# Optimization experiments

Hardware: AMD Instinct MI355X
Metric: run time of the kernel (lower is better)

Reference implementation:

```python
import jax, jax.numpy as jnp
import numpy as np

V = 10000   # vocab_size
L = 12      # n_layer
H = 12      # n_head
C = 768     # n_embd
TE = 64     # t_embd
WTE = C - TE
BS = 1024   # block_size
B, T = 4, 1024
D = C // H
EPS = 1e-5


def setup_inputs() -> dict:
    key = jax.random.key(0)
    ks = jax.random.split(key, 12)
    s = 0.02
    def n(k, shape, extra=1.0):
        return jax.random.normal(k, shape, jnp.float32) * (s * extra)
    resid_scale = 1.0 / np.sqrt(2 * L)  # c_proj init std scaling from _init_weights loop
    return {
        'idx': jax.random.randint(ks[0], (B, T), 0, V),
        'ts': jax.random.uniform(ks[1], (B, T), jnp.float32) * 100.0,
        'wte': n(ks[2], (V, WTE)),
        'basis_freq': jnp.asarray(1.0 / 10 ** np.linspace(0, 9, TE), jnp.float32),
        'phase': jnp.zeros((TE,), jnp.float32),
        'wpe': n(ks[3], (BS, C)),
        'ln1_w': jnp.ones((L, C), jnp.float32), 'ln1_b': jnp.zeros((L, C), jnp.float32),
        'qkv_w': n(ks[4], (L, 3 * C, C)), 'qkv_b': jnp.zeros((L, 3 * C), jnp.float32),
        'proj_w': n(ks[5], (L, C, C), resid_scale), 'proj_b': jnp.zeros((L, C), jnp.float32),
        'ln2_w': jnp.ones((L, C), jnp.float32), 'ln2_b': jnp.zeros((L, C), jnp.float32),
        'fc_w': n(ks[6], (L, 4 * C, C)), 'fc_b': jnp.zeros((L, 4 * C), jnp.float32),
        'fc2_w': n(ks[7], (L, C, 4 * C), resid_scale), 'fc2_b': jnp.zeros((L, C), jnp.float32),
        'lnf_w': jnp.ones((C,), jnp.float32), 'lnf_b': jnp.zeros((C,), jnp.float32),
        'lm_w': n(ks[8], (V, C)),
        'tp_w': n(ks[9], (1, C)),
    }


def _ln(x, w, b):
    mu = jnp.mean(x, -1, keepdims=True)
    var = jnp.mean((x - mu) ** 2, -1, keepdims=True)
    return (x - mu) * jax.lax.rsqrt(var + EPS) * w + b


def reference(idx, ts, wte, basis_freq, phase, wpe, ln1_w, ln1_b, qkv_w, qkv_b,
              proj_w, proj_b, ln2_w, ln2_b, fc_w, fc_b, fc2_w, fc2_b,
              lnf_w, lnf_b, lm_w, tp_w):
    Bv, Tv = idx.shape
    tok = wte[idx]                                      # [B,T,C-TE]
    tim = jnp.cos(ts[..., None] * basis_freq + phase)   # TimeEncode -> [B,T,TE]
    x = jnp.concatenate([tok, tim], axis=-1) + wpe[:Tv]
    mask = jnp.tril(jnp.ones((Tv, Tv), bool))
    scale = 1.0 / np.sqrt(D)

    def block(x, p):
        l1w, l1b, qw, qb, pw, pb, l2w, l2b, fw, fb, f2w, f2b = p
        h = _ln(x, l1w, l1b)
        qkv = h @ qw.T + qb                              # [B,T,3C]
        q, k, v = jnp.split(qkv, 3, axis=-1)
        def heads(z):
            return z.reshape(Bv, Tv, H, D).transpose(0, 2, 1, 3)  # [B,H,T,D]
        q, k, v = heads(q), heads(k), heads(v)
        att = jnp.einsum('bhtd,bhsd->bhts', q, k) * scale
        att = jnp.where(mask, att, -jnp.inf)             # causal masked_fill
        att = jax.nn.softmax(att, axis=-1)
        y = jnp.einsum('bhts,bhsd->bhtd', att, v)
        y = y.transpose(0, 2, 1, 3).reshape(Bv, Tv, C)
        x = x + (y @ pw.T + pb)
        h2 = _ln(x, l2w, l2b)
        m = jax.nn.gelu(h2 @ fw.T + fb, approximate=False)  # torch nn.GELU default is exact
        x = x + (m @ f2w.T + f2b)
        return x, None

    x, _ = jax.lax.scan(block, x, (ln1_w, ln1_b, qkv_w, qkv_b, proj_w, proj_b,
                                   ln2_w, ln2_b, fc_w, fc_b, fc2_w, fc2_b))
    x = _ln(x, lnf_w, lnf_b)
    logits = x @ lm_w.T          # [B,T,V]
    tpred = x @ tp_w.T           # [B,T,1]
    return logits, tpred
```

## Files before the change

kernel.cpp:

```cpp
#include <hip/hip_runtime.h>
#include <hip/hip_bf16.h>
#include <math.h>

#define Bb   4
#define Tt   1024
#define Cc   768
#define Hh   12
#define Dd   64
#define Ll   12
#define Vv   10000
#define WTEe 704
#define MTOT 4096

#define QSCALE 0.18033688f

typedef __bf16 bf16x8 __attribute__((ext_vector_type(8)));
typedef float  f32x4  __attribute__((ext_vector_type(4)));
typedef unsigned short u16;

typedef const __attribute__((address_space(1))) void* gptr_t;
typedef __attribute__((address_space(3))) void* lptr_t;

__device__ inline void gload16(const void* g, void* l) {
    __builtin_amdgcn_global_load_lds((gptr_t)g, (lptr_t)l, 16, 0, 0);
}

__device__ inline u16 f2bf(float f) {
    unsigned int u = __float_as_uint(f);
    return (u16)((u + 0x7fffu + ((u >> 16) & 1u)) >> 16);
}
__device__ inline float bf2f(u16 u) { return __uint_as_float(((unsigned)u) << 16); }

__device__ inline float gelu_f(float v) {
    float t = v * (0.797884561f + 0.0356774081f * v * v);
    float e = __expf(2.f * t);
    float th = 1.f - 2.f / (e + 1.f);
    return 0.5f * v * (1.f + th);
}

#if __has_builtin(__builtin_amdgcn_exp2f)
__device__ inline float fast_exp2(float x) { return __builtin_amdgcn_exp2f(x); }
#else
__device__ inline float fast_exp2(float x) { return exp2f(x); }
#endif

#define WAITVM(N)  asm volatile("s_waitcnt vmcnt(" #N ")" ::: "memory")
#define WAITLGKM0() asm volatile("s_waitcnt lgkmcnt(0)" ::: "memory")
#define SCHEDB()   __builtin_amdgcn_sched_barrier(0)
#define SBAR()     __builtin_amdgcn_s_barrier()

__global__ __launch_bounds__(256)
void convert_pack(const float* __restrict__ in, u16* __restrict__ out,
                  int nk8, int K, int rowmod, int scaleLim)
{
    int i = blockIdx.x * 256 + threadIdx.x;
    if (i >= nk8) return;
    int row = (i << 3) / K;
    int col = (i << 3) % K;
    float s = 1.f;
    if (rowmod && (row % rowmod) < scaleLim) s = QSCALE;
    float4 v0 = ((const float4*)in)[2 * i];
    float4 v1 = ((const float4*)in)[2 * i + 1];
    uint4 o;
    o.x = (unsigned)f2bf(v0.x * s) | ((unsigned)f2bf(v0.y * s) << 16);
    o.y = (unsigned)f2bf(v0.z * s) | ((unsigned)f2bf(v0.w * s) << 16);
    o.z = (unsigned)f2bf(v1.x * s) | ((unsigned)f2bf(v1.y * s) << 16);
    o.w = (unsigned)f2bf(v1.z * s) | ((unsigned)f2bf(v1.w * s) << 16);
    int tile = row >> 4, kt = col >> 5;
    int l = (row & 15) | (((col >> 3) & 3) << 4);
    size_t off = (((size_t)tile * (K >> 5) + kt) << 9) + l * 8;
    *(uint4*)(out + off) = o;
}

__global__ __launch_bounds__(256)
void scale_qkvb(const float* __restrict__ in, float* __restrict__ out, int n)
{
    int i = blockIdx.x * 256 + threadIdx.x;
    if (i >= n) return;
    int col = i % (3 * Cc);
    out[i] = in[i] * (col < Cc ? QSCALE : 1.f);
}

__global__ __launch_bounds__(256)
void embed_kernel(const int* __restrict__ idx, const float* __restrict__ ts,
                  const float* __restrict__ wte, const float* __restrict__ freq,
                  const float* __restrict__ ph, const float* __restrict__ wpe,
                  float* __restrict__ x)
{
    const int bt  = blockIdx.x;
    const int t   = bt & (Tt - 1);
    const int tok = idx[bt];
    const float tv = ts[bt];
#pragma unroll
    for (int j = 0; j < 3; ++j) {
        int c = threadIdx.x + (j << 8);
        float val;
        if (c < WTEe) val = wte[(size_t)tok * WTEe + c];
        else {
            int e = c - WTEe;
            val = cosf(tv * freq[e] + ph[e]);
        }
        x[(size_t)bt * Cc + c] = val + wpe[(size_t)t * Cc + c];
    }
}

__global__ __launch_bounds__(256)
void ln_pack16(const float* __restrict__ x, const float* __restrict__ wt,
               const float* __restrict__ bs, u16* __restrict__ out)
{
    __shared__ float mus[16], rss[16];
    const int tid  = threadIdx.x;
    const int lane = tid & 63;
    const int w    = tid >> 6;
    const int tile = blockIdx.x;
    const int r0   = tile << 4;

#pragma unroll
    for (int rr = 0; rr < 4; ++rr) {
        const int row = r0 + w * 4 + rr;
        const float* xr = x + (size_t)row * Cc;
        float s = 0.f, s2 = 0.f;
#pragma unroll
        for (int j = 0; j < 12; ++j) {
            float v = xr[lane + (j << 6)];
            s += v; s2 += v * v;
        }
#pragma unroll
        for (int m = 32; m; m >>= 1) {
            s  += __shfl_xor(s, m);
            s2 += __shfl_xor(s2, m);
        }
        if (lane == 0) {
            float mu = s * (1.f / 768.f);
            float var = s2 * (1.f / 768.f) - mu * mu;
            mus[w * 4 + rr] = mu;
            rss[w * 4 + rr] = rsqrtf(var + 1e-5f);
        }
    }
    __syncthreads();

    u16* ob = out + ((size_t)tile * 24 << 9);
#pragma unroll
    for (int it = 0; it < 6; ++it) {
        int c   = tid + (it << 8);
        int kt  = c >> 6, l = c & 63;
        int row = l & 15, g = l >> 4;
        int col = kt * 32 + g * 8;
        float mu = mus[row], rs = rss[row];
        const float* xp = x + (size_t)(r0 + row) * Cc + col;
        float4 a = *(const float4*)xp;
        float4 bq = *(const float4*)(xp + 4);
        ushort o[8];
        o[0] = f2bf((a.x - mu) * rs * wt[col]     + bs[col]);
        o[1] = f2bf((a.y - mu) * rs * wt[col + 1] + bs[col + 1]);
        o[2] = f2bf((a.z - mu) * rs * wt[col + 2] + bs[col + 2]);
        o[3] = f2bf((a.w - mu) * rs * wt[col + 3] + bs[col + 3]);
        o[4] = f2bf((bq.x - mu) * rs * wt[col + 4] + bs[col + 4]);
        o[5] = f2bf((bq.y - mu) * rs * wt[col + 5] + bs[col + 5]);
        o[6] = f2bf((bq.z - mu) * rs * wt[col + 6] + bs[col + 6]);
        o[7] = f2bf((bq.w - mu) * rs * wt[col + 7] + bs[col + 7]);
        *(uint4*)(ob + ((size_t)kt << 9) + l * 8) = *(uint4*)o;
    }
}

__device__ inline void st_out(float* p, size_t o, float v) { p[o] = v; }
__device__ inline void st_out(u16*   p, size_t o, float v) { p[o] = f2bf(v); }

template<int EPI, int APK, typename OutT>
__global__ __launch_bounds__(256)
void gemm_bf16(const u16* __restrict__ A, const u16* __restrict__ Wp,
               const float* __restrict__ bias, const float* __restrict__ resid,
               OutT* __restrict__ out, u16* __restrict__ vt, int N, int K)
{
    __shared__ uint4 AF[3][8][64];
    __shared__ uint4 BF[3][8][64];
    const int tid  = threadIdx.x;
    const int lane = tid & 63;
    const int w    = tid >> 6;
    const int wr   = w >> 1, wc = w & 1;
    const int lq   = lane & 15, g = lane >> 4;
    const int m0   = blockIdx.x * 128, n0 = blockIdx.y * 128;
    const int KB   = K >> 5;

    const u16 *ap0, *ap1;
    if (APK) {
        ap0 = A + ((((size_t)(m0 >> 4) + 2 * w) * KB) << 9) + lane * 8;
        ap1 = ap0 + ((size_t)KB << 9);
    } else {
        ap0 = A + (size_t)(m0 + (2 * w) * 16 + lq) * K + g * 8;
        ap1 = ap0 + (size_t)16 * K;
    }

    int tn0 = (n0 >> 4) + 2 * w, tn1 = tn0 + 1;
    const int tmax = (N >> 4) - 1;
    tn0 = tn0 < tmax ? tn0 : tmax;
    tn1 = tn1 < tmax ? tn1 : tmax;
    const u16* bq0 = Wp + (((size_t)tn0 * KB) << 9) + lane * 8;
    const u16* bq1 = Wp + (((size_t)tn1 * KB) << 9) + lane * 8;

    f32x4 acc[4][4] = {};
    const int nk = KB;

#define GSTAGE(s, sl) do {                                               \
        if (APK) {                                                       \
            gload16(ap0 + ((size_t)(s) << 9), &AF[sl][2 * w][lane]);     \
            gload16(ap1 + ((size_t)(s) << 9), &AF[sl][2 * w + 1][lane]); \
        } else {                                                         \
            gload16(ap0 + ((s) << 5), &AF[sl][2 * w][lane]);             \
            gload16(ap1 + ((s) << 5), &AF[sl][2 * w + 1][lane]);         \
        }                                                                \
        gload16(bq0 + ((size_t)(s) << 9), &BF[sl][2 * w][lane]);         \
        gload16(bq1 + ((size_t)(s) << 9), &BF[sl][2 * w + 1][lane]); } while (0)

    GSTAGE(0, 0);
    GSTAGE(1, 1);
    WAITVM(4);
    SCHEDB();
    SBAR();
    SCHEDB();

    int sl = 0;
    for (int t = 0; t < nk; ++t) {
        int sl2 = sl + 2; if (sl2 >= 3) sl2 -= 3;
        if (t + 2 < nk) GSTAGE(t + 2, sl2);

        bf16x8 af[4], bfr[4];
#pragma unroll
        for (int mi = 0; mi < 4; ++mi)
            af[mi] = __builtin_bit_cast(bf16x8, AF[sl][wr * 4 + mi][lane]);
#pragma unroll
        for (int ni = 0; ni < 4; ++ni)
            bfr[ni] = __builtin_bit_cast(bf16x8, BF[sl][wc * 4 + ni][lane]);
        __builtin_amdgcn_s_setprio(1);
#pragma unroll
        for (int mi = 0; mi < 4; ++mi)
#pragma unroll
            for (int ni = 0; ni < 4; ++ni)
                acc[mi][ni] = __builtin_amdgcn_mfma_f32_16x16x32_bf16(
                    af[mi], bfr[ni], acc[mi][ni], 0, 0, 0);
        __builtin_amdgcn_s_setprio(0);

        if (t + 2 < nk) { WAITVM(4); }
        else           { WAITVM(0); }
        SCHEDB();
        SBAR();
        SCHEDB();
        sl = (sl + 1 == 3) ? 0 : sl + 1;
    }
#undef GSTAGE

    if (EPI == 3 && n0 >= 1536) {
#pragma unroll
        for (int mi = 0; mi < 4; ++mi)
#pragma unroll
            for (int ni = 0; ni < 4; ++ni) {
                int col = n0 + wc * 64 + ni * 16 + lq;
                int c2  = col - 1536;
                int hh  = c2 >> 6, dd = c2 & 63;
                int row = m0 + wr * 64 + mi * 16 + g * 4;
                int bb  = row >> 10, tr = row & 1023;
                float bv = bias[col];
                ushort4 o;
                o.x = f2bf(acc[mi][ni][0] + bv);
                o.y = f2bf(acc[mi][ni][1] + bv);
                o.z = f2bf(acc[mi][ni][2] + bv);
                o.w = f2bf(acc[mi][ni][3] + bv);
                *(ushort4*)&vt[(((size_t)bb * Hh + hh) * Dd + dd) * Tt + tr] = o;
            }
        return;
    }

#pragma unroll
    for (int mi = 0; mi < 4; ++mi)
#pragma unroll
        for (int ni = 0; ni < 4; ++ni) {
            int col = n0 + wc * 64 + ni * 16 + lq;
            if (col >= N) continue;
            int row = m0 + wr * 64 + mi * 16 + g * 4;
            float bv = bias ? bias[col] : 0.f;
#pragma unroll
            for (int q = 0; q < 4; ++q) {
                float v = acc[mi][ni][q] + bv;
                size_t o = (size_t)(row + q) * N + col;
                if (EPI == 1) v += resid[o];
                if (EPI == 2) v = gelu_f(v);
                st_out(out, o, v);
            }
        }
}

template<int EPI, typename OutT>
__global__ __launch_bounds__(256)
void gemm_n64(const u16* __restrict__ A, const u16* __restrict__ Wp,
              const float* __restrict__ bias, const float* __restrict__ resid,
              OutT* __restrict__ out, int N, int K)
{
    __shared__ uint4 AF[2][8][64];
    __shared__ uint4 BF[2][16][64];
    const int tid  = threadIdx.x;
    const int lane = tid & 63;
    const int w    = tid >> 6;
    const int wr   = w & 1, wc = w >> 1;
    const int lq   = lane & 15, g = lane >> 4;
    const int m0   = blockIdx.x * 64, n0 = blockIdx.y * 128;
    const int KB   = K >> 5;
    const int nk   = K >> 6;

    const u16* ap = A + (size_t)(m0 + w * 16 + lq) * K + g * 8;
    int tn0 = (n0 >> 4) + 2 * w, tn1 = tn0 + 1;
    const int tmax = (N >> 4) - 1;
    tn0 = tn0 < tmax ? tn0 : tmax;
    tn1 = tn1 < tmax ? tn1 : tmax;
    const u16* bq0 = Wp + (((size_t)tn0 * KB) << 9) + lane * 8;
    const u16* bq1 = Wp + (((size_t)tn1 * KB) << 9) + lane * 8;

    f32x4 acc[2][4] = {};

#define GSTAGE(t, bi) do {                                                 \
        gload16(ap + ((t) << 6),      &AF[bi][2 * w][lane]);               \
        gload16(ap + ((t) << 6) + 32, &AF[bi][2 * w + 1][lane]);           \
        gload16(bq0 + ((size_t)(2 * (t)) << 9),     &BF[bi][4 * w][lane]); \
        gload16(bq0 + ((size_t)(2 * (t) + 1) << 9), &BF[bi][4 * w + 1][lane]); \
        gload16(bq1 + ((size_t)(2 * (t)) << 9),     &BF[bi][4 * w + 2][lane]); \
        gload16(bq1 + ((size_t)(2 * (t) + 1) << 9), &BF[bi][4 * w + 3][lane]); } while (0)

    GSTAGE(0, 0);
    WAITVM(0);
    SCHEDB();
    SBAR();
    SCHEDB();

    for (int t = 0; t < nk; ++t) {
        const int buf = t & 1;
        if (t + 1 < nk) GSTAGE(t + 1, buf ^ 1);

#pragma unroll
        for (int s = 0; s < 2; ++s) {
            bf16x8 a0 = __builtin_bit_cast(bf16x8, AF[buf][(wr * 2) * 2 + s][lane]);
            bf16x8 a1 = __builtin_bit_cast(bf16x8, AF[buf][(wr * 2 + 1) * 2 + s][lane]);
            bf16x8 bb[4];
#pragma unroll
            for (int ni = 0; ni < 4; ++ni)
                bb[ni] = __builtin_bit_cast(bf16x8, BF[buf][(wc * 4 + ni) * 2 + s][lane]);
            __builtin_amdgcn_s_setprio(1);
#pragma unroll
            for (int ni = 0; ni < 4; ++ni) {
                acc[0][ni] = __builtin_amdgcn_mfma_f32_16x16x32_bf16(
                    a0, bb[ni], acc[0][ni], 0, 0, 0);
                acc[1][ni] = __builtin_amdgcn_mfma_f32_16x16x32_bf16(
                    a1, bb[ni], acc[1][ni], 0, 0, 0);
            }
            __builtin_amdgcn_s_setprio(0);
        }

        WAITVM(0);
        SCHEDB();
        SBAR();
        SCHEDB();
    }
#undef GSTAGE

#pragma unroll
    for (int mi = 0; mi < 2; ++mi)
#pragma unroll
        for (int ni = 0; ni < 4; ++ni) {
            int col = n0 + wc * 64 + ni * 16 + lq;
            if (col >= N) continue;
            int row = m0 + (wr * 2 + mi) * 16 + g * 4;
            float bv = bias ? bias[col] : 0.f;
#pragma unroll
            for (int q = 0; q < 4; ++q) {
                float v = acc[mi][ni][q] + bv;
                size_t o = (size_t)(row + q) * N + col;
                if (EPI == 1) v += resid[o];
                if (EPI == 2) v = gelu_f(v);
                st_out(out, o, v);
            }
        }
}

template<int EPI, typename OutT>
__global__ __launch_bounds__(512, 2)
void gemm8p(const u16* __restrict__ Apk, const u16* __restrict__ Wp,
            const float* __restrict__ bias, const float* __restrict__ resid,
            OutT* __restrict__ out, int N, int K)
{
    __shared__ uint4 AF[2][16][2][64];
    __shared__ uint4 BF[2][16][2][64];
    const int tid  = threadIdx.x;
    const int lane = tid & 63;
    const int w    = tid >> 6;
    const int wr   = w >> 2, wc = w & 3;
    const int lq   = lane & 15, g = lane >> 4;
    const int m0   = blockIdx.x * 256, n0 = blockIdx.y * 256;
    const int KB   = K >> 5;

    const u16* aq0 = Apk + ((((size_t)(m0 >> 4) + 2 * w) * KB) << 9) + lane * 8;
    const u16* aq1 = aq0 + ((size_t)KB << 9);

    int tn0 = (n0 >> 4) + 2 * w, tn1 = tn0 + 1;
    const int tmax = (N >> 4) - 1;
    tn0 = tn0 < tmax ? tn0 : tmax;
    tn1 = tn1 < tmax ? tn1 : tmax;
    const u16* bq0 = Wp + (((size_t)tn0 * KB) << 9) + lane * 8;
    const u16* bq1 = Wp + (((size_t)tn1 * KB) << 9) + lane * 8;

    f32x4 acc[8][4] = {};
    const int nt = K >> 6;

    gload16(aq0,       &AF[0][2 * w][0][lane]);
    gload16(aq1,       &AF[0][2 * w + 1][0][lane]);
    gload16(bq0,       &BF[0][2 * w][0][lane]);
    gload16(bq1,       &BF[0][2 * w + 1][0][lane]);
    gload16(aq0 + 512, &AF[0][2 * w][1][lane]);
    gload16(aq1 + 512, &AF[0][2 * w + 1][1][lane]);
    gload16(bq0 + 512, &BF[0][2 * w][1][lane]);
    gload16(bq1 + 512, &BF[0][2 * w + 1][1][lane]);
    WAITVM(0);
    SCHEDB();
    SBAR();

    int buf = 0;
    for (int t = 0; t < nt; ++t) {
        const bool more = (t + 1 < nt);
        const size_t bb0 = (size_t)(2 * (t + 1)) << 9;
        bf16x8 a0[4], a1[4], b0[4];

#pragma unroll
        for (int i = 0; i < 4; ++i)
            a0[i] = __builtin_bit_cast(bf16x8, AF[buf][wr * 8 + i][0][lane]);
#pragma unroll
        for (int i = 0; i < 4; ++i)
            b0[i] = __builtin_bit_cast(bf16x8, BF[buf][wc * 4 + i][0][lane]);
        if (more) {
            gload16(aq0 + bb0, &AF[buf ^ 1][2 * w][0][lane]);
            gload16(aq1 + bb0, &AF[buf ^ 1][2 * w + 1][0][lane]);
        }
        SCHEDB();
        SBAR();
        WAITLGKM0();
        SCHEDB();
        __builtin_amdgcn_s_setprio(1);
#pragma unroll
        for (int mi = 0; mi < 4; ++mi)
#pragma unroll
            for (int ni = 0; ni < 4; ++ni)
                acc[mi][ni] = __builtin_amdgcn_mfma_f32_16x16x32_bf16(
                    a0[mi], b0[ni], acc[mi][ni], 0, 0, 0);
        __builtin_amdgcn_s_setprio(0);
        SBAR();

#pragma unroll
        for (int i = 0; i < 4; ++i)
            a1[i] = __builtin_bit_cast(bf16x8, AF[buf][wr * 8 + 4 + i][0][lane]);
        if (more) {
            gload16(bq0 + bb0, &BF[buf ^ 1][2 * w][0][lane]);
            gload16(bq1 + bb0, &BF[buf ^ 1][2 * w + 1][0][lane]);
        }
        SCHEDB();
        SBAR();
        WAITLGKM0();
        SCHEDB();
        __builtin_amdgcn_s_setprio(1);
#pragma unroll
        for (int mi = 0; mi < 4; ++mi)
#pragma unroll
            for (int ni = 0; ni < 4; ++ni)
                acc[4 + mi][ni] = __builtin_amdgcn_mfma_f32_16x16x32_bf16(
                    a1[mi], b0[ni], acc[4 + mi][ni], 0, 0, 0);
        __builtin_amdgcn_s_setprio(0);
        if (more) { WAITVM(4); } else { WAITVM(0); }
        SCHEDB();
        SBAR();

#pragma unroll
        for (int i = 0; i < 4; ++i)
            a0[i] = __builtin_bit_cast(bf16x8, AF[buf][wr * 8 + i][1][lane]);
#pragma unroll
        for (int i = 0; i < 4; ++i)
            b0[i] = __builtin_bit_cast(bf16x8, BF[buf][wc * 4 + i][1][lane]);
        if (more) {
            gload16(aq0 + bb0 + 512, &AF[buf ^ 1][2 * w][1][lane]);
            gload16(aq1 + bb0 + 512, &AF[buf ^ 1][2 * w + 1][1][lane]);
        }
        SCHEDB();
        SBAR();
        WAITLGKM0();
        SCHEDB();
        __builtin_amdgcn_s_setprio(1);
#pragma unroll
        for (int mi = 0; mi < 4; ++mi)
#pragma unroll
            for (int ni = 0; ni < 4; ++ni)
                acc[mi][ni] = __builtin_amdgcn_mfma_f32_16x16x32_bf16(
                    a0[mi], b0[ni], acc[mi][ni], 0, 0, 0);
        __builtin_amdgcn_s_setprio(0);
        SBAR();

#pragma unroll
        for (int i = 0; i < 4; ++i)
            a1[i] = __builtin_bit_cast(bf16x8, AF[buf][wr * 8 + 4 + i][1][lane]);
        if (more) {
            gload16(bq0 + bb0 + 512, &BF[buf ^ 1][2 * w][1][lane]);
            gload16(bq1 + bb0 + 512, &BF[buf ^ 1][2 * w + 1][1][lane]);
        }
        SCHEDB();
        SBAR();
        WAITLGKM0();
        SCHEDB();
        __builtin_amdgcn_s_setprio(1);
#pragma unroll
        for (int mi = 0; mi < 4; ++mi)
#pragma unroll
            for (int ni = 0; ni < 4; ++ni)
                acc[4 + mi][ni] = __builtin_amdgcn_mfma_f32_16x16x32_bf16(
                    a1[mi], b0[ni], acc[4 + mi][ni], 0, 0, 0);
        __builtin_amdgcn_s_setprio(0);
        if (more) { WAITVM(4); } else { WAITVM(0); }
        SCHEDB();
        SBAR();

        buf ^= 1;
    }

#pragma unroll
    for (int mi = 0; mi < 8; ++mi)
#pragma unroll
        for (int ni = 0; ni < 4; ++ni) {
            int col = n0 + wc * 64 + ni * 16 + lq;
            if (col >= N) continue;
            int row = m0 + wr * 128 + mi * 16 + g * 4;
            float bv = bias ? bias[col] : 0.f;
#pragma unroll
            for (int q = 0; q < 4; ++q) {
                float v = acc[mi][ni][q] + bv;
                size_t o = (size_t)(row + q) * N + col;
                if (EPI == 1) v += resid[o];
                if (EPI == 2) v = gelu_f(v);
                st_out(out, o, v);
            }
        }
}

__global__ __launch_bounds__(512)
void attn_mfma(const u16* __restrict__ qkv, const u16* __restrict__ vt,
               u16* __restrict__ y)
{
    __shared__ uint4 KF[2][4][2][64];
    __shared__ uint4 VF[2][4][2][64];

    const int tid  = threadIdx.x;
    const int lane = tid & 63;
    const int w    = tid >> 6;
    const int lq   = lane & 15, g = lane >> 4;
    const int m    = gridDim.x - 1 - blockIdx.x;
    const int bh   = blockIdx.y;
    const int b    = bh / Hh, h = bh % Hh;
    const int wq0  = m * 128 + w * 16;
    const size_t base = (size_t)b * Tt * (3 * Cc);

    const u16* qrow = qkv + base + (size_t)(wq0 + lq) * (3 * Cc) + h * Dd;
    bf16x8 qf0 = __builtin_bit_cast(bf16x8, *(const uint4*)(qrow + g * 8));
    bf16x8 qf1 = __builtin_bit_cast(bf16x8, *(const uint4*)(qrow + 32 + g * 8));

    f32x4 yac[4] = {};
    float lrun = 0.f;

    const int wm = w & 3;
    const u16* kbase = qkv + base + Cc + h * Dd + (size_t)(wm * 16 + lq) * (3 * Cc) + g * 8;
    const u16* vbase = vt + ((size_t)bh * Dd + wm * 16 + lq) * Tt + g * 8;

#define STAGE(c, bi)  do {                                              \
        if (w < 4) {                                                    \
            const u16* kp = kbase + (size_t)(c) * 64 * (3 * Cc);        \
            gload16(kp,      &KF[bi][wm][0][lane]);                     \
            gload16(kp + 32, &KF[bi][wm][1][lane]);                     \
        } else {                                                        \
            const u16* vp = vbase + (c) * 64;                           \
            gload16(vp,      &VF[bi][wm][0][lane]);                     \
            gload16(vp + 32, &VF[bi][wm][1][lane]);                     \
        }                                                               \
    } while (0)

    const int nch = 2 * m + 2;
    STAGE(0, 0);
    WAITVM(0);
    SCHEDB();
    SBAR();

    const int srcb = lq + ((g & 1) << 5);

    int buf = 0;
    for (int c = 0; c < nch; ++c) {
        if (c + 1 < nch) STAGE(c + 1, buf ^ 1);

        f32x4 sc[4] = {};
        __builtin_amdgcn_s_setprio(1);
#pragma unroll
        for (int nt = 0; nt < 4; ++nt) {
            bf16x8 k0 = __builtin_bit_cast(bf16x8, KF[buf][nt][0][lane]);
            bf16x8 k1 = __builtin_bit_cast(bf16x8, KF[buf][nt][1][lane]);
            sc[nt] = __builtin_amdgcn_mfma_f32_16x16x32_bf16(k0, qf0, sc[nt], 0, 0, 0);
            sc[nt] = __builtin_amdgcn_mfma_f32_16x16x32_bf16(k1, qf1, sc[nt], 0, 0, 0);
        }
        __builtin_amdgcn_s_setprio(0);

        const int s0 = c * 64;
        if (s0 + 63 > wq0) {
            const int qg = wq0 + lq;
#pragma unroll
            for (int nt = 0; nt < 4; ++nt) {
                const int kb = s0 + nt * 16 + (g << 2);
#pragma unroll
                for (int j = 0; j < 4; ++j)
                    if (kb + j > qg) sc[nt][j] = -1e30f;
            }
        }

        float ls = 0.f;
#pragma unroll
        for (int nt = 0; nt < 4; ++nt)
#pragma unroll
            for (int j = 0; j < 4; ++j) {
                float p = fast_exp2(sc[nt][j]);
                sc[nt][j] = p;
                ls += p;
            }
        ls += __shfl_xor(ls, 16);
        ls += __shfl_xor(ls, 32);
        lrun += ls;

        unsigned pk[4][2];
#pragma unroll
        for (int nt = 0; nt < 4; ++nt) {
            unsigned u0 = __float_as_uint(sc[nt][0]);
            unsigned u1 = __float_as_uint(sc[nt][1]);
            unsigned u2 = __float_as_uint(sc[nt][2]);
            unsigned u3 = __float_as_uint(sc[nt][3]);
            pk[nt][0] = (u0 >> 16) | (u1 & 0xffff0000u);
            pk[nt][1] = (u2 >> 16) | (u3 & 0xffff0000u);
        }

        unsigned pa0[4], pa1[4];
#pragma unroll
        for (int m2 = 0; m2 < 4; ++m2) {
            int hsel = m2 & 1;
            int src  = srcb + ((m2 >> 1) << 4);
            unsigned lo0 = __shfl(pk[0][hsel], src);
            unsigned hi0 = __shfl(pk[1][hsel], src);
            unsigned lo1 = __shfl(pk[2][hsel], src);
            unsigned hi1 = __shfl(pk[3][hsel], src);
            pa0[m2] = (g >> 1) ? hi0 : lo0;
            pa1[m2] = (g >> 1) ? hi1 : lo1;
        }
        uint4 A0 = make_uint4(pa0[0], pa0[1], pa0[2], pa0[3]);
        uint4 A1 = make_uint4(pa1[0], pa1[1], pa1[2], pa1[3]);
        bf16x8 pA0 = __builtin_bit_cast(bf16x8, A0);
        bf16x8 pA1 = __builtin_bit_cast(bf16x8, A1);

        __builtin_amdgcn_s_setprio(1);
#pragma unroll
        for (int dt = 0; dt < 4; ++dt) {
            bf16x8 vb0 = __builtin_bit_cast(bf16x8, VF[buf][dt][0][lane]);
            bf16x8 vb1 = __builtin_bit_cast(bf16x8, VF[buf][dt][1][lane]);
            yac[dt] = __builtin_amdgcn_mfma_f32_16x16x32_bf16(pA0, vb0, yac[dt], 0, 0, 0);
            yac[dt] = __builtin_amdgcn_mfma_f32_16x16x32_bf16(pA1, vb1, yac[dt], 0, 0, 0);
        }
        __builtin_amdgcn_s_setprio(0);

        if (c + 1 < nch) { WAITVM(0); }
        SCHEDB();
        SBAR();
        buf ^= 1;
    }
#undef STAGE

    f32x4 rl;
#pragma unroll
    for (int j = 0; j < 4; ++j)
        rl[j] = 1.0f / __shfl(lrun, (g << 2) + j);
#pragma unroll
    for (int dt = 0; dt < 4; ++dt)
#pragma unroll
        for (int j = 0; j < 4; ++j)
            y[(size_t)(b * Tt + wq0 + (g << 2) + j) * Cc + h * Dd + dt * 16 + lq]
                = f2bf(yac[dt][j] * rl[j]);
}

__global__ __launch_bounds__(256)
void tpred_kernel(const u16* __restrict__ hp, const float* __restrict__ tp,
                  float* __restrict__ out)
{
    const int row  = blockIdx.x * 4 + (threadIdx.x >> 6);
    const int lane = threadIdx.x & 63;
    const int tile = row >> 4, r15 = row & 15;
    const u16* tb = hp + ((size_t)tile * 24 << 9);
    float s = 0.f;
#pragma unroll
    for (int j = 0; j < 12; ++j) {
        int col = lane + (j << 6);
        int kt = col >> 5, g = (col >> 3) & 3, e = col & 7;
        s += bf2f(tb[((size_t)kt << 9) + (r15 | (g << 4)) * 8 + e]) * tp[col];
    }
#pragma unroll
    for (int m = 32; m; m >>= 1) s += __shfl_xor(s, m);
    if (lane == 0) out[row] = s;
}

extern "C" void kernel_launch(void* const* d_in, const int* in_sizes, int n_in,
                              void* d_out, int out_size, void* d_ws, size_t ws_size,
                              hipStream_t stream)
{
    const int*   idx  = (const int*)d_in[0];
    const float* ts   = (const float*)d_in[1];
    const float* wte  = (const float*)d_in[2];
    const float* freq = (const float*)d_in[3];
    const float* ph   = (const float*)d_in[4];
    const float* wpe  = (const float*)d_in[5];
    const float* ln1w = (const float*)d_in[6];
    const float* ln1b = (const float*)d_in[7];
    const float* qkvw = (const float*)d_in[8];
    const float* qkvb = (const float*)d_in[9];
    const float* pw   = (const float*)d_in[10];
    const float* pb   = (const float*)d_in[11];
    const float* ln2w = (const float*)d_in[12];
    const float* ln2b = (const float*)d_in[13];
    const float* fcw  = (const float*)d_in[14];
    const float* fcb  = (const float*)d_in[15];
    const float* f2w  = (const float*)d_in[16];
    const float* f2b  = (const float*)d_in[17];
    const float* lnfw = (const float*)d_in[18];
    const float* lnfb = (const float*)d_in[19];
    const float* lmw  = (const float*)d_in[20];
    const float* tpw  = (const float*)d_in[21];
    float* out = (float*)d_out;

    const int n_qkvw = 3 * Cc * Cc, n_pw = Cc * Cc, n_fcw = 4 * Cc * Cc;

    char* p = (char*)d_ws;
    float* x    = (float*)p;               p += (size_t)MTOT * Cc * 4;
    u16*   qkvB = (u16*)p;                 p += (size_t)MTOT * 3 * Cc * 2;
    u16*   VtB  = (u16*)p;                 p += (size_t)Bb * Hh * Dd * Tt * 2;
    u16*   hB   = (u16*)p;                 p += (size_t)MTOT * Cc * 2;
    u16*   yB   = (u16*)p;                 p += (size_t)MTOT * Cc * 2;
    u16*   mbB  = (u16*)p;                 p += (size_t)MTOT * 4 * Cc * 2;
    u16*   lmwB = (u16*)p;                 p += (size_t)Vv * Cc * 2;
    float* sbias= (float*)p;               p += (size_t)Ll * 3 * Cc * 4;
    char* wbase = p;

    size_t need_big = (size_t)(wbase - (char*)d_ws)
                    + ((size_t)Ll * (n_qkvw + n_pw + 2 * n_fcw)) * 2;
    bool big = ws_size >= need_big;

    u16 *wqA, *wpA, *wfA, *wf2A;
    if (big) {
        wqA  = (u16*)wbase;                wbase += (size_t)Ll * n_qkvw * 2;
        wpA  = (u16*)wbase;                wbase += (size_t)Ll * n_pw * 2;
        wfA  = (u16*)wbase;                wbase += (size_t)Ll * n_fcw * 2;
        wf2A = (u16*)wbase;
    } else {
        wqA  = (u16*)wbase;                wbase += (size_t)n_qkvw * 2;
        wpA  = (u16*)wbase;                wbase += (size_t)n_pw * 2;
        wfA  = (u16*)wbase;                wbase += (size_t)n_fcw * 2;
        wf2A = (u16*)wbase;
    }

    auto pack = [&](const float* src, u16* dst, size_t rows, int K,
                    int rowmod, int scaleLim) {
        int nk8 = (int)(rows * K / 8);
        convert_pack<<<(nk8 + 255) / 256, 256, 0, stream>>>(
            src, dst, nk8, K, rowmod, scaleLim);
    };

    pack(lmw, lmwB, Vv, Cc, 0, 0);
    {
        int nb = Ll * 3 * Cc;
        scale_qkvb<<<(nb + 255) / 256, 256, 0, stream>>>(qkvb, sbias, nb);
    }
    if (big) {
        pack(qkvw, wqA,  (size_t)Ll * 3 * Cc, Cc, 3 * Cc, Cc);
        pack(pw,   wpA,  (size_t)Ll * Cc,     Cc, 0, 0);
        pack(fcw,  wfA,  (size_t)Ll * 4 * Cc, Cc, 0, 0);
        pack(f2w,  wf2A, (size_t)Ll * Cc, 4 * Cc, 0, 0);
    }
    embed_kernel<<<MTOT, 256, 0, stream>>>(idx, ts, wte, freq, ph, wpe, x);

    for (int l = 0; l < Ll; ++l) {
        u16 *wqB, *wpB, *wfB, *wf2B;
        if (big) {
            wqB  = wqA  + (size_t)l * n_qkvw;
            wpB  = wpA  + (size_t)l * n_pw;
            wfB  = wfA  + (size_t)l * n_fcw;
            wf2B = wf2A + (size_t)l * n_fcw;
        } else {
            wqB = wqA; wpB = wpA; wfB = wfA; wf2B = wf2A;
            pack(qkvw + (size_t)l * n_qkvw, wqB, 3 * Cc, Cc, 3 * Cc, Cc);
            pack(pw   + (size_t)l * n_pw,   wpB, Cc,     Cc, 0, 0);
            pack(fcw  + (size_t)l * n_fcw,  wfB, 4 * Cc, Cc, 0, 0);
            pack(f2w  + (size_t)l * n_fcw,  wf2B, Cc, 4 * Cc, 0, 0);
        }

        ln_pack16<<<MTOT / 16, 256, 0, stream>>>(x, ln1w + l * Cc, ln1b + l * Cc, hB);
        gemm_bf16<3, 1, u16><<<dim3(32, 18), 256, 0, stream>>>(
            hB, wqB, sbias + (size_t)l * 3 * Cc, nullptr, qkvB, VtB, 3 * Cc, Cc);
        attn_mfma<<<dim3(Tt / 128, Bb * Hh), 512, 0, stream>>>(qkvB, VtB, yB);
        gemm_n64<1, float><<<dim3(64, 6), 256, 0, stream>>>(
            yB, wpB, pb + (size_t)l * Cc, x, x, Cc, Cc);
        ln_pack16<<<MTOT / 16, 256, 0, stream>>>(x, ln2w + l * Cc, ln2b + l * Cc, hB);
        gemm_bf16<2, 1, u16><<<dim3(32, 24), 256, 0, stream>>>(
            hB, wfB, fcb + (size_t)l * 4 * Cc, nullptr, mbB, nullptr, 4 * Cc, Cc);
        gemm_n64<1, float><<<dim3(64, 6), 256, 0, stream>>>(
            mbB, wf2B, f2b + (size_t)l * Cc, x, x, Cc, 4 * Cc);
    }

    ln_pack16<<<MTOT / 16, 256, 0, stream>>>(x, lnfw, lnfb, hB);
    gemm8p<0, float><<<dim3(16, 40), 512, 0, stream>>>(
        hB, lmwB, nullptr, nullptr, out, Vv, Cc);
    tpred_kernel<<<MTOT / 4, 256, 0, stream>>>(hB, tpw, out + (size_t)MTOT * Vv);
}
```

Baseline: 2.451 ms.

## Use 64-row M tiles with 64-wide K steps for QKV and FC GEMMs

The two GEMM kernels are merged into one templated kernel with a 64x128 output tile, double-buffered 64-wide K stages, and optional packed-A input. The QKV and FC GEMMs now use this smaller tile, doubling their grid size from 128x128 tiles with a 3-stage pipeline. The goal is more blocks for better CU occupancy and load balance, at the cost of less operand reuse per block and a shallower prefetch pipeline.

```diff
diff --git a/kernel.cpp b/kernel.cpp
--- a/kernel.cpp
+++ b/kernel.cpp
@@ -168,28 +168,24 @@
 
 template<int EPI, int APK, typename OutT>
 __global__ __launch_bounds__(256)
-void gemm_bf16(const u16* __restrict__ A, const u16* __restrict__ Wp,
+void gemm_nk64(const u16* __restrict__ A, const u16* __restrict__ Wp,
                const float* __restrict__ bias, const float* __restrict__ resid,
                OutT* __restrict__ out, u16* __restrict__ vt, int N, int K)
 {
-    __shared__ uint4 AF[3][8][64];
-    __shared__ uint4 BF[3][8][64];
+    __shared__ uint4 AF[2][8][64];
+    __shared__ uint4 BF[2][16][64];
     const int tid  = threadIdx.x;
     const int lane = tid & 63;
     const int w    = tid >> 6;
-    const int wr   = w >> 1, wc = w & 1;
+    const int wr   = w & 1, wc = w >> 1;
     const int lq   = lane & 15, g = lane >> 4;
-    const int m0   = blockIdx.x * 128, n0 = blockIdx.y * 128;
+    const int m0   = blockIdx.x * 64, n0 = blockIdx.y * 128;
     const int KB   = K >> 5;
-
-    const u16 *ap0, *ap1;
-    if (APK) {
-        ap0 = A + ((((size_t)(m0 >> 4) + 2 * w) * KB) << 9) + lane * 8;
-        ap1 = ap0 + ((size_t)KB << 9);
-    } else {
-        ap0 = A + (size_t)(m0 + (2 * w) * 16 + lq) * K + g * 8;
-        ap1 = ap0 + (size_t)16 * K;
-    }
+    const int nk   = K >> 6;
+
+    const u16* ap;
+    if (APK) ap = A + ((((size_t)(m0 >> 4) + w) * KB) << 9) + lane * 8;
+    else     ap = A + (size_t)(m0 + w * 16 + lq) * K + g * 8;
 
     int tn0 = (n0 >> 4) + 2 * w, tn1 = tn0 + 1;
     const int tmax = (N >> 4) - 1;
@@ -198,66 +194,66 @@
     const u16* bq0 = Wp + (((size_t)tn0 * KB) << 9) + lane * 8;
     const u16* bq1 = Wp + (((size_t)tn1 * KB) << 9) + lane * 8;
 
-    f32x4 acc[4][4] = {};
-    const int nk = KB;
-
-#define GSTAGE(s, sl) do {                                               \
-        if (APK) {                                                       \
-            gload16(ap0 + ((size_t)(s) << 9), &AF[sl][2 * w][lane]);     \
-            gload16(ap1 + ((size_t)(s) << 9), &AF[sl][2 * w + 1][lane]); \
-        } else {                                                         \
-            gload16(ap0 + ((s) << 5), &AF[sl][2 * w][lane]);             \
-            gload16(ap1 + ((s) << 5), &AF[sl][2 * w + 1][lane]);         \
-        }                                                                \
-        gload16(bq0 + ((size_t)(s) << 9), &BF[sl][2 * w][lane]);         \
-        gload16(bq1 + ((size_t)(s) << 9), &BF[sl][2 * w + 1][lane]); } while (0)
+    f32x4 acc[2][4] = {};
+
+#define GSTAGE(t, bi) do {                                                 \
+        if (APK) {                                                         \
+            gload16(ap + ((size_t)(2 * (t)) << 9),     &AF[bi][2 * w][lane]); \
+            gload16(ap + ((size_t)(2 * (t) + 1) << 9), &AF[bi][2 * w + 1][lane]); \
+        } else {                                                           \
+            gload16(ap + ((t) << 6),      &AF[bi][2 * w][lane]);           \
+            gload16(ap + ((t) << 6) + 32, &AF[bi][2 * w + 1][lane]);       \
+        }                                                                  \
+        gload16(bq0 + ((size_t)(2 * (t)) << 9),     &BF[bi][4 * w][lane]); \
+        gload16(bq0 + ((size_t)(2 * (t) + 1) << 9), &BF[bi][4 * w + 1][lane]); \
+        gload16(bq1 + ((size_t)(2 * (t)) << 9),     &BF[bi][4 * w + 2][lane]); \
+        gload16(bq1 + ((size_t)(2 * (t) + 1) << 9), &BF[bi][4 * w + 3][lane]); } while (0)
 
     GSTAGE(0, 0);
-    GSTAGE(1, 1);
-    WAITVM(4);
+    WAITVM(0);
     SCHEDB();
     SBAR();
     SCHEDB();
 
-    int sl = 0;
     for (int t = 0; t < nk; ++t) {
-        int sl2 = sl + 2; if (sl2 >= 3) sl2 -= 3;
-        if (t + 2 < nk) GSTAGE(t + 2, sl2);
-
-        bf16x8 af[4], bfr[4];
-#pragma unroll
-        for (int mi = 0; mi < 4; ++mi)
-            af[mi] = __builtin_bit_cast(bf16x8, AF[sl][wr * 4 + mi][lane]);
-#pragma unroll
-        for (int ni = 0; ni < 4; ++ni)
-            bfr[ni] = __builtin_bit_cast(bf16x8, BF[sl][wc * 4 + ni][lane]);
-        __builtin_amdgcn_s_setprio(1);
-#pragma unroll
-        for (int mi = 0; mi < 4; ++mi)
+        const int buf = t & 1;
+        if (t + 1 < nk) GSTAGE(t + 1, buf ^ 1);
+
+#pragma unroll
+        for (int s = 0; s < 2; ++s) {
+            bf16x8 a0 = __builtin_bit_cast(bf16x8, AF[buf][(wr * 2) * 2 + s][lane]);
+            bf16x8 a1 = __builtin_bit_cast(bf16x8, AF[buf][(wr * 2 + 1) * 2 + s][lane]);
+            bf16x8 bb[4];
 #pragma unroll
             for (int ni = 0; ni < 4; ++ni)
-                acc[mi][ni] = __builtin_amdgcn_mfma_f32_16x16x32_bf16(
-                    af[mi], bfr[ni], acc[mi][ni], 0, 0, 0);
-        __builtin_amdgcn_s_setprio(0);
-
-        if (t + 2 < nk) { WAITVM(4); }
-        else           { WAITVM(0); }
-        SCHEDB();
-        SBAR();
-        SCHEDB();
-        sl = (sl + 1 == 3) ? 0 : sl + 1;
+                bb[ni] = __builtin_bit_cast(bf16x8, BF[buf][(wc * 4 + ni) * 2 + s][lane]);
+            __builtin_amdgcn_s_setprio(1);
+#pragma unroll
+            for (int ni = 0; ni < 4; ++ni) {
+                acc[0][ni] = __builtin_amdgcn_mfma_f32_16x16x32_bf16(
+                    a0, bb[ni], acc[0][ni], 0, 0, 0);
+                acc[1][ni] = __builtin_amdgcn_mfma_f32_16x16x32_bf16(
+                    a1, bb[ni], acc[1][ni], 0, 0, 0);
+            }
+            __builtin_amdgcn_s_setprio(0);
+        }
+
+        WAITVM(0);
+        SCHEDB();
+        SBAR();
+        SCHEDB();
     }
 #undef GSTAGE
 
     if (EPI == 3 && n0 >= 1536) {
 #pragma unroll
-        for (int mi = 0; mi < 4; ++mi)
+        for (int mi = 0; mi < 2; ++mi)
 #pragma unroll
             for (int ni = 0; ni < 4; ++ni) {
                 int col = n0 + wc * 64 + ni * 16 + lq;
                 int c2  = col - 1536;
                 int hh  = c2 >> 6, dd = c2 & 63;
-                int row = m0 + wr * 64 + mi * 16 + g * 4;
+                int row = m0 + (wr * 2 + mi) * 16 + g * 4;
                 int bb  = row >> 10, tr = row & 1023;
                 float bv = bias[col];
                 ushort4 o;
@@ -269,96 +265,6 @@
             }
         return;
     }
-
-#pragma unroll
-    for (int mi = 0; mi < 4; ++mi)
-#pragma unroll
-        for (int ni = 0; ni < 4; ++ni) {
-            int col = n0 + wc * 64 + ni * 16 + lq;
-            if (col >= N) continue;
-            int row = m0 + wr * 64 + mi * 16 + g * 4;
-            float bv = bias ? bias[col] : 0.f;
-#pragma unroll
-            for (int q = 0; q < 4; ++q) {
-                float v = acc[mi][ni][q] + bv;
-                size_t o = (size_t)(row + q) * N + col;
-                if (EPI == 1) v += resid[o];
-                if (EPI == 2) v = gelu_f(v);
-                st_out(out, o, v);
-            }
-        }
-}
-
-template<int EPI, typename OutT>
-__global__ __launch_bounds__(256)
-void gemm_n64(const u16* __restrict__ A, const u16* __restrict__ Wp,
-              const float* __restrict__ bias, const float* __restrict__ resid,
-              OutT* __restrict__ out, int N, int K)
-{
-    __shared__ uint4 AF[2][8][64];
-    __shared__ uint4 BF[2][16][64];
-    const int tid  = threadIdx.x;
-    const int lane = tid & 63;
-    const int w    = tid >> 6;
-    const int wr   = w & 1, wc = w >> 1;
-    const int lq   = lane & 15, g = lane >> 4;
-    const int m0   = blockIdx.x * 64, n0 = blockIdx.y * 128;
-    const int KB   = K >> 5;
-    const int nk   = K >> 6;
-
-    const u16* ap = A + (size_t)(m0 + w * 16 + lq) * K + g * 8;
-    int tn0 = (n0 >> 4) + 2 * w, tn1 = tn0 + 1;
-    const int tmax = (N >> 4) - 1;
-    tn0 = tn0 < tmax ? tn0 : tmax;
-    tn1 = tn1 < tmax ? tn1 : tmax;
-    const u16* bq0 = Wp + (((size_t)tn0 * KB) << 9) + lane * 8;
-    const u16* bq1 = Wp + (((size_t)tn1 * KB) << 9) + lane * 8;
-
-    f32x4 acc[2][4] = {};
-
-#define GSTAGE(t, bi) do {                                                 \
-        gload16(ap + ((t) << 6),      &AF[bi][2 * w][lane]);               \
-        gload16(ap + ((t) << 6) + 32, &AF[bi][2 * w + 1][lane]);           \
-        gload16(bq0 + ((size_t)(2 * (t)) << 9),     &BF[bi][4 * w][lane]); \
-        gload16(bq0 + ((size_t)(2 * (t) + 1) << 9), &BF[bi][4 * w + 1][lane]); \
-        gload16(bq1 + ((size_t)(2 * (t)) << 9),     &BF[bi][4 * w + 2][lane]); \
-        gload16(bq1 + ((size_t)(2 * (t) + 1) << 9), &BF[bi][4 * w + 3][lane]); } while (0)
-
-    GSTAGE(0, 0);
-    WAITVM(0);
-    SCHEDB();
-    SBAR();
-    SCHEDB();
-
-    for (int t = 0; t < nk; ++t) {
-        const int buf = t & 1;
-        if (t + 1 < nk) GSTAGE(t + 1, buf ^ 1);
-
-#pragma unroll
-        for (int s = 0; s < 2; ++s) {
-            bf16x8 a0 = __builtin_bit_cast(bf16x8, AF[buf][(wr * 2) * 2 + s][lane]);
-            bf16x8 a1 = __builtin_bit_cast(bf16x8, AF[buf][(wr * 2 + 1) * 2 + s][lane]);
-            bf16x8 bb[4];
-#pragma unroll
-            for (int ni = 0; ni < 4; ++ni)
-                bb[ni] = __builtin_bit_cast(bf16x8, BF[buf][(wc * 4 + ni) * 2 + s][lane]);
-            __builtin_amdgcn_s_setprio(1);
-#pragma unroll
-            for (int ni = 0; ni < 4; ++ni) {
-                acc[0][ni] = __builtin_amdgcn_mfma_f32_16x16x32_bf16(
-                    a0, bb[ni], acc[0][ni], 0, 0, 0);
-                acc[1][ni] = __builtin_amdgcn_mfma_f32_16x16x32_bf16(
-                    a1, bb[ni], acc[1][ni], 0, 0, 0);
-            }
-            __builtin_amdgcn_s_setprio(0);
-        }
-
-        WAITVM(0);
-        SCHEDB();
-        SBAR();
-        SCHEDB();
-    }
-#undef GSTAGE
 
 #pragma unroll
     for (int mi = 0; mi < 2; ++mi)
@@ -801,16 +707,16 @@
         }
 
         ln_pack16<<<MTOT / 16, 256, 0, stream>>>(x, ln1w + l * Cc, ln1b + l * Cc, hB);
-        gemm_bf16<3, 1, u16><<<dim3(32, 18), 256, 0, stream>>>(
+        gemm_nk64<3, 1, u16><<<dim3(64, 18), 256, 0, stream>>>(
             hB, wqB, sbias + (size_t)l * 3 * Cc, nullptr, qkvB, VtB, 3 * Cc, Cc);
         attn_mfma<<<dim3(Tt / 128, Bb * Hh), 512, 0, stream>>>(qkvB, VtB, yB);
-        gemm_n64<1, float><<<dim3(64, 6), 256, 0, stream>>>(
-            yB, wpB, pb + (size_t)l * Cc, x, x, Cc, Cc);
+        gemm_nk64<1, 0, float><<<dim3(64, 6), 256, 0, stream>>>(
+            yB, wpB, pb + (size_t)l * Cc, x, x, nullptr, Cc, Cc);
         ln_pack16<<<MTOT / 16, 256, 0, stream>>>(x, ln2w + l * Cc, ln2b + l * Cc, hB);
-        gemm_bf16<2, 1, u16><<<dim3(32, 24), 256, 0, stream>>>(
+        gemm_nk64<2, 1, u16><<<dim3(64, 24), 256, 0, stream>>>(
             hB, wfB, fcb + (size_t)l * 4 * Cc, nullptr, mbB, nullptr, 4 * Cc, Cc);
-        gemm_n64<1, float><<<dim3(64, 6), 256, 0, stream>>>(
-            mbB, wf2B, f2b + (size_t)l * Cc, x, x, Cc, 4 * Cc);
+        gemm_nk64<1, 0, float><<<dim3(64, 6), 256, 0, stream>>>(
+            mbB, wf2B, f2b + (size_t)l * Cc, x, x, nullptr, Cc, 4 * Cc);
     }
 
     ln_pack16<<<MTOT / 16, 256, 0, stream>>>(x, lnfw, lnfb, hB);
```

Result: slower. 2.576 ms (+5.1%).
